# Kernel tuning notes

Hardware: AMD Instinct MI355X
Metric: run time of the kernel (lower is better)

The kernel has to match this reference:

```python
import jax, jax.numpy as jnp
import numpy as np

N = 100000
E = 1600000
F_IN = 32
HID = 16
C_OUT = 10
K = 4


def setup_inputs() -> dict:
    key = jax.random.key(0)
    k1, k2, k3, k4, k5, k6, k7 = jax.random.split(key, 7)
    x = jax.random.normal(k1, (N, F_IN), dtype=jnp.float32)
    edge_index = jax.random.randint(k2, (2, E), 0, N, dtype=jnp.int64)
    # ChebConv weights: one [in, out] matrix per Chebyshev order k
    W1 = jax.random.normal(k3, (K, F_IN, HID), dtype=jnp.float32) / np.sqrt(F_IN)
    b1 = jax.random.normal(k4, (HID,), dtype=jnp.float32) * 0.01
    W2 = jax.random.normal(k5, (K, HID, C_OUT), dtype=jnp.float32) / np.sqrt(HID)
    b2 = jax.random.normal(k6, (C_OUT,), dtype=jnp.float32) * 0.01
    return {"x": x, "edge_index": edge_index, "W1": W1, "b1": b1, "W2": W2, "b2": b2}


def _cheb_conv(h, src, dst, norm, W, b, num_nodes):
    # Tx_0 = h; Tx_1 = L_hat h; Tx_k = 2 L_hat Tx_{k-1} - Tx_{k-2}
    def prop(v):  # v: [N, F] -> L_hat v via sparse gather/scatter
        return jax.ops.segment_sum(norm[:, None] * v[src], dst, num_segments=num_nodes)

    Tx0 = h
    out = Tx0 @ W[0]
    Tx1 = prop(h)
    out = out + Tx1 @ W[1]
    for k in range(2, W.shape[0]):
        Tx2 = 2.0 * prop(Tx1) - Tx0
        out = out + Tx2 @ W[k]
        Tx0, Tx1 = Tx1, Tx2
    return out + b


def reference(x, edge_index, W1, b1, W2, b2):
    src, dst = edge_index[0], edge_index[1]
    num_nodes = x.shape[0]
    # symmetric normalization with lambda_max = 2: L_hat = -D^{-1/2} A D^{-1/2}
    deg = jax.ops.segment_sum(jnp.ones((src.shape[0],), dtype=x.dtype), dst, num_segments=num_nodes)
    dis = jnp.where(deg > 0, jax.lax.rsqrt(jnp.maximum(deg, 1.0)), 0.0)
    norm = -dis[src] * dis[dst]
    h = _cheb_conv(x, src, dst, norm, W1, b1, num_nodes)
    h = jax.nn.relu(h)
    # dropout is identity in eval mode
    h = _cheb_conv(h, src, dst, norm, W2, b2, num_nodes)
    return jax.nn.log_softmax(h, axis=1)
```

## Files before the change

### kernel.cpp

```cpp
#include <hip/hip_runtime.h>
#include <hip/hip_bf16.h>
#include <math.h>


#define BLK 256
#define BLKP 512
#define NBUCK_MAX 256
#define CHUNK 8192
#define CAPB 16384
#define PLACE_CAP 10240

__device__ inline unsigned short f32_to_bf16_rne(float f) {
    unsigned int u = __float_as_uint(f);
    unsigned int rounding = 0x7FFFu + ((u >> 16) & 1u);
    return (unsigned short)((u + rounding) >> 16);
}
__device__ inline unsigned int pack_bf16x2(float a, float b) {
    return (unsigned int)f32_to_bf16_rne(a) | ((unsigned int)f32_to_bf16_rne(b) << 16);
}
__device__ inline void unpack8(const uint4 u, float* f) {
    const unsigned int* p = &u.x;
#pragma unroll
    for (int j = 0; j < 4; j++) {
        unsigned int w = p[j];
        f[2 * j]     = __uint_as_float(w << 16);
        f[2 * j + 1] = __uint_as_float(w & 0xFFFF0000u);
    }
}
__device__ inline void add8(const uint4 u, float* acc) {
    const unsigned int* p = &u.x;
#pragma unroll
    for (int j = 0; j < 4; j++) {
        unsigned int w = p[j];
        acc[2 * j]     += __uint_as_float(w << 16);
        acc[2 * j + 1] += __uint_as_float(w & 0xFFFF0000u);
    }
}
__device__ inline uint4 pack8(const float* r) {
    uint4 o;
    o.x = pack_bf16x2(r[0], r[1]);
    o.y = pack_bf16x2(r[2], r[3]);
    o.z = pack_bf16x2(r[4], r[5]);
    o.w = pack_bf16x2(r[6], r[7]);
    return o;
}

__device__ inline void fma8_w8(const uint4 u, float s, const float* __restrict__ W,
                               float* acc) {
    const unsigned int* p = &u.x;
#pragma unroll
    for (int q = 0; q < 4; q++) {
        float fa = __uint_as_float(p[q] << 16) * s;
        float fb = __uint_as_float(p[q] & 0xFFFF0000u) * s;
        const float* Wa = W + (2 * q) * 16;
        const float* Wb = W + (2 * q + 1) * 16;
#pragma unroll
        for (int j = 0; j < 8; j++) acc[j] += fa * Wa[j] + fb * Wb[j];
    }
}
__device__ inline void fma8_w10(const uint4 u, float s, const float* __restrict__ W,
                                float* acc) {
    const unsigned int* p = &u.x;
#pragma unroll
    for (int q = 0; q < 4; q++) {
        float fa = __uint_as_float(p[q] << 16) * s;
        float fb = __uint_as_float(p[q] & 0xFFFF0000u) * s;
        const float* Wa = W + (2 * q) * 10;
        const float* Wb = W + (2 * q + 1) * 10;
#pragma unroll
        for (int j = 0; j < 10; j++) acc[j] += fa * Wa[j] + fb * Wb[j];
    }
}

__global__ __launch_bounds__(BLK)
void binned_scatter_kernel(const int* __restrict__ src, const int* __restrict__ dst,
                           int* __restrict__ bfill, int* __restrict__ tmp,
                           int E, int nbuck) {
    __shared__ int cnt[NBUCK_MAX];
    __shared__ int lofs[NBUCK_MAX + 1];
    __shared__ int pos[NBUCK_MAX];
    __shared__ int gbase[NBUCK_MAX];
    __shared__ int stage[CHUNK];
    __shared__ unsigned char bkt[CHUNK];

    int tid = threadIdx.x;
    int e0 = blockIdx.x * CHUNK;
    int nE = min(CHUNK, E - e0);

    for (int b = tid; b < nbuck; b += BLK) { cnt[b] = 0; pos[b] = 0; }
    __syncthreads();

    for (int i = tid; i < nE; i += BLK) {
        int d = dst[e0 + i];
        atomicAdd(&cnt[d >> 9], 1);
    }
    __syncthreads();

    {
        int v = (tid < nbuck) ? cnt[tid] : 0;
        lofs[tid] = v;
        __syncthreads();
        for (int off = 1; off < BLK; off <<= 1) {
            int t = (tid >= off) ? lofs[tid - off] : 0;
            __syncthreads();
            lofs[tid] += t;
            __syncthreads();
        }
        int incl = lofs[tid];
        __syncthreads();
        lofs[tid] = incl - v;
        if (tid == 0) lofs[nbuck] = nE;
        if (tid < nbuck && v > 0)
            gbase[tid] = tid * CAPB + atomicAdd(&bfill[tid], v);
    }
    __syncthreads();

    for (int i = tid; i < nE; i += BLK) {
        int s = src[e0 + i];
        int d = dst[e0 + i];
        int b = d >> 9;
        int slot = lofs[b] + atomicAdd(&pos[b], 1);
        stage[slot] = (s << 9) | (d & 511);
        bkt[slot] = (unsigned char)b;
    }
    __syncthreads();

    for (int i = tid; i < nE; i += BLK) {
        int b = bkt[i];
        tmp[gbase[b] + (i - lofs[b])] = stage[i];
    }
}

__global__ __launch_bounds__(BLKP)
void bucket_place_kernel(const int* __restrict__ bfill, const int* __restrict__ tmp,
                         int* __restrict__ psrc, int* __restrict__ rowbeg,
                         int* __restrict__ rowend, float* __restrict__ dis,
                         float* __restrict__ d2, float* __restrict__ inv,
                         const float* __restrict__ x, uint4* __restrict__ u0, int N) {
    __shared__ int cnt4[512 * 4];
    __shared__ int ofs[512];
    __shared__ int fill4[512 * 4];
    __shared__ int stage[PLACE_CAP];

    int b = blockIdx.x;
    int tid = threadIdx.x;
    int n0 = b << 9;
    int nn = min(512, N - n0);
    int S = b * CAPB;
    int tot = bfill[b];

    int t1 = N >> 2, t2 = N >> 1, t3 = t2 + t1;

    for (int i = tid; i < 512 * 4; i += BLKP) { cnt4[i] = 0; fill4[i] = 0; }
    __syncthreads();

    for (int i = tid; i < tot; i += BLKP) {
        int rec = tmp[S + i];
        int nl = rec & 511;
        int s = rec >> 9;
        int q = (s >= t2) ? ((s >= t3) ? 3 : 2) : ((s >= t1) ? 1 : 0);
        atomicAdd(&cnt4[nl * 4 + q], 1);
    }
    __syncthreads();

    int c0 = cnt4[tid * 4 + 0], c1 = cnt4[tid * 4 + 1];
    int c2 = cnt4[tid * 4 + 2], c3 = cnt4[tid * 4 + 3];
    int v = c0 + c1 + c2 + c3;
    cnt4[tid * 4 + 0] = 0;
    cnt4[tid * 4 + 1] = c0;
    cnt4[tid * 4 + 2] = c0 + c1;
    cnt4[tid * 4 + 3] = c0 + c1 + c2;
    ofs[tid] = v;
    __syncthreads();
    for (int off = 1; off < 512; off <<= 1) {
        int t = (tid >= off) ? ofs[tid - off] : 0;
        __syncthreads();
        ofs[tid] += t;
        __syncthreads();
    }
    int excl = ofs[tid] - v;
    __syncthreads();
    ofs[tid] = excl;
    float dn = (v > 0) ? rsqrtf((float)v) : 0.0f;
    if (tid < nn) {
        int n = n0 + tid;
        rowbeg[n] = S + excl;
        rowend[n] = S + excl + v;
        float fv = (float)v;
        dis[n] = dn;
        d2[n]  = (v > 0) ? 1.0f / fv : 0.0f;
        inv[n] = (v > 0) ? sqrtf(fv) : 0.0f;
        const float4* xr = reinterpret_cast<const float4*>(x + (size_t)n * 32);
#pragma unroll
        for (int c = 0; c < 4; c++) {
            float4 a = xr[c * 2], bb = xr[c * 2 + 1];
            float r[8] = {dn * a.x, dn * a.y, dn * a.z, dn * a.w,
                          dn * bb.x, dn * bb.y, dn * bb.z, dn * bb.w};
            u0[(size_t)n * 4 + c] = pack8(r);
        }
    }
    __syncthreads();

    if (tot <= PLACE_CAP) {
        for (int i = tid; i < tot; i += BLKP) {
            int rec = tmp[S + i];
            int nl = rec & 511;
            int s = rec >> 9;
            int q = (s >= t2) ? ((s >= t3) ? 3 : 2) : ((s >= t1) ? 1 : 0);
            int slot = ofs[nl] + cnt4[nl * 4 + q] + atomicAdd(&fill4[nl * 4 + q], 1);
            stage[slot] = s;
        }
        __syncthreads();
        for (int i = tid; i < tot; i += BLKP) psrc[S + i] = stage[i];
    } else {
        for (int i = tid; i < tot; i += BLKP) {
            int rec = tmp[S + i];
            int nl = rec & 511;
            int s = rec >> 9;
            int q = (s >= t2) ? ((s >= t3) ? 3 : 2) : ((s >= t1) ? 1 : 0);
            int slot = S + ofs[nl] + cnt4[nl * 4 + q] + atomicAdd(&fill4[nl * 4 + q], 1);
            psrc[slot] = s;
        }
    }
}

template <int C, bool HAVE_PREV>
__global__ __launch_bounds__(BLK)
void prop_u_kernel(const int* __restrict__ rowbeg, const int* __restrict__ rowend,
                   const int* __restrict__ psrc, const float* __restrict__ d2,
                   const uint4* __restrict__ vb, const uint4* __restrict__ prevb,
                   uint4* __restrict__ outb, float scale, int N) {
    int t = blockIdx.x * blockDim.x + threadIdx.x;
    int n = t / C;
    int c = t % C;
    if (n >= N) return;
    int beg = rowbeg[n];
    int end = rowend[n];
    float acc[8];
#pragma unroll
    for (int j = 0; j < 8; j++) acc[j] = 0.f;
    int i = beg;
    for (; i + 7 < end; i += 8) {
        int s0 = psrc[i],     s1 = psrc[i + 1], s2 = psrc[i + 2], s3 = psrc[i + 3];
        int s4 = psrc[i + 4], s5 = psrc[i + 5], s6 = psrc[i + 6], s7 = psrc[i + 7];
        uint4 a0 = vb[(size_t)s0 * C + c];
        uint4 a1 = vb[(size_t)s1 * C + c];
        uint4 a2 = vb[(size_t)s2 * C + c];
        uint4 a3 = vb[(size_t)s3 * C + c];
        uint4 a4 = vb[(size_t)s4 * C + c];
        uint4 a5 = vb[(size_t)s5 * C + c];
        uint4 a6 = vb[(size_t)s6 * C + c];
        uint4 a7 = vb[(size_t)s7 * C + c];
        add8(a0, acc); add8(a1, acc); add8(a2, acc); add8(a3, acc);
        add8(a4, acc); add8(a5, acc); add8(a6, acc); add8(a7, acc);
    }
    for (; i + 3 < end; i += 4) {
        int s0 = psrc[i], s1 = psrc[i + 1], s2 = psrc[i + 2], s3 = psrc[i + 3];
        uint4 a0 = vb[(size_t)s0 * C + c];
        uint4 a1 = vb[(size_t)s1 * C + c];
        uint4 a2 = vb[(size_t)s2 * C + c];
        uint4 a3 = vb[(size_t)s3 * C + c];
        add8(a0, acc); add8(a1, acc); add8(a2, acc); add8(a3, acc);
    }
    for (; i < end; i++) {
        uint4 a0 = vb[(size_t)psrc[i] * C + c];
        add8(a0, acc);
    }
    float f = -scale * d2[n];
    float r[8];
    if (HAVE_PREV) {
        float p[8];
        unpack8(prevb[(size_t)n * C + c], p);
#pragma unroll
        for (int j = 0; j < 8; j++) r[j] = f * acc[j] - p[j];
    } else {
#pragma unroll
        for (int j = 0; j < 8; j++) r[j] = f * acc[j];
    }
    outb[(size_t)n * C + c] = pack8(r);
}

__global__ __launch_bounds__(BLK)
void combine1_kernel(const float* __restrict__ x, const uint4* __restrict__ u1,
                     const uint4* __restrict__ u2, const uint4* __restrict__ u3,
                     const float* __restrict__ inv, const float* __restrict__ dis,
                     const float* __restrict__ W1, const float* __restrict__ b1,
                     uint4* __restrict__ hb, uint4* __restrict__ uh, int N) {
    __shared__ float sW[4 * 32 * 16];
    __shared__ float sb[16];
    for (int i = threadIdx.x; i < 4 * 32 * 16; i += blockDim.x) sW[i] = W1[i];
    if (threadIdx.x < 16) sb[threadIdx.x] = b1[threadIdx.x];
    __syncthreads();
    int t = blockIdx.x * blockDim.x + threadIdx.x;
    int n = t >> 1;
    int h = t & 1;
    if (n >= N) return;
    const float* sWh = sW + h * 8;
    float acc[8];
#pragma unroll
    for (int j = 0; j < 8; j++) acc[j] = sb[h * 8 + j];
    {
        const float4* in4 = reinterpret_cast<const float4*>(x + (size_t)n * 32);
#pragma unroll
        for (int q = 0; q < 8; q++) {
            float4 a = in4[q];
            const float* Wq = sWh + q * 4 * 16;
#pragma unroll
            for (int j = 0; j < 8; j++)
                acc[j] += a.x * Wq[j] + a.y * Wq[16 + j] + a.z * Wq[32 + j] + a.w * Wq[48 + j];
        }
    }
    float iv = inv[n];
#pragma unroll
    for (int c = 0; c < 4; c++) fma8_w8(u1[(size_t)n * 4 + c], iv, sWh + 512 + c * 128, acc);
#pragma unroll
    for (int c = 0; c < 4; c++) fma8_w8(u2[(size_t)n * 4 + c], iv, sWh + 1024 + c * 128, acc);
#pragma unroll
    for (int c = 0; c < 4; c++) fma8_w8(u3[(size_t)n * 4 + c], iv, sWh + 1536 + c * 128, acc);
    if (iv == 0.0f) {
        const float4* in4 = reinterpret_cast<const float4*>(x + (size_t)n * 32);
#pragma unroll
        for (int q = 0; q < 8; q++) {
            float4 a = in4[q];
            const float* Wq = sWh + 1024 + q * 4 * 16;
#pragma unroll
            for (int j = 0; j < 8; j++)
                acc[j] -= a.x * Wq[j] + a.y * Wq[16 + j] + a.z * Wq[32 + j] + a.w * Wq[48 + j];
        }
    }
    float dn = dis[n];
    float r[8], u[8];
#pragma unroll
    for (int j = 0; j < 8; j++) {
        r[j] = fmaxf(acc[j], 0.0f);
        u[j] = dn * r[j];
    }
    hb[(size_t)n * 2 + h] = pack8(r);
    uh[(size_t)n * 2 + h] = pack8(u);
}

__global__ __launch_bounds__(BLK)
void combine2_kernel(const uint4* __restrict__ hb, const uint4* __restrict__ us1,
                     const uint4* __restrict__ us2, const uint4* __restrict__ us3,
                     const float* __restrict__ inv,
                     const float* __restrict__ W2, const float* __restrict__ b2,
                     float* __restrict__ out, int N) {
    __shared__ float sW[4 * 16 * 10];
    __shared__ float sb[10];
    for (int i = threadIdx.x; i < 4 * 16 * 10; i += blockDim.x) sW[i] = W2[i];
    if (threadIdx.x < 10) sb[threadIdx.x] = b2[threadIdx.x];
    __syncthreads();
    int n = blockIdx.x * blockDim.x + threadIdx.x;
    if (n >= N) return;
    float acc[10];
#pragma unroll
    for (int c = 0; c < 10; c++) acc[c] = sb[c];
    float iv = inv[n];
#pragma unroll
    for (int c = 0; c < 2; c++) fma8_w10(hb[(size_t)n * 2 + c],  1.0f, sW + c * 80, acc);
#pragma unroll
    for (int c = 0; c < 2; c++) fma8_w10(us1[(size_t)n * 2 + c], iv, sW + 160 + c * 80, acc);
#pragma unroll
    for (int c = 0; c < 2; c++) fma8_w10(us2[(size_t)n * 2 + c], iv, sW + 320 + c * 80, acc);
#pragma unroll
    for (int c = 0; c < 2; c++) fma8_w10(us3[(size_t)n * 2 + c], iv, sW + 480 + c * 80, acc);
    if (iv == 0.0f) {
#pragma unroll
        for (int c = 0; c < 2; c++) fma8_w10(hb[(size_t)n * 2 + c], -1.0f, sW + 320 + c * 80, acc);
    }
    float m = acc[0];
#pragma unroll
    for (int c = 1; c < 10; c++) m = fmaxf(m, acc[c]);
    float sum = 0.0f;
#pragma unroll
    for (int c = 0; c < 10; c++) sum += expf(acc[c] - m);
    float lse = m + logf(sum);
    float* o = out + (size_t)n * 10;
#pragma unroll
    for (int c = 0; c < 10; c++) o[c] = acc[c] - lse;
}

extern "C" void kernel_launch(void* const* d_in, const int* in_sizes, int n_in,
                              void* d_out, int out_size, void* d_ws, size_t ws_size,
                              hipStream_t stream) {
    const float* x  = (const float*)d_in[0];
    const int*   ei = (const int*)d_in[1];
    const float* W1 = (const float*)d_in[2];
    const float* b1 = (const float*)d_in[3];
    const float* W2 = (const float*)d_in[4];
    const float* b2 = (const float*)d_in[5];
    float* out = (float*)d_out;

    const int N = in_sizes[0] / 32;
    const int E = in_sizes[1] / 2;
    const int* src = ei;
    const int* dst = ei + E;

    const int nbuck = (N + 511) / 512;

    char* w = (char*)d_ws;
    int*   bfill  = (int*)w;              w += NBUCK_MAX * 4;
    int*   rowbeg = (int*)w;              w += (size_t)(N + 4) * 4;
    int*   rowend = (int*)w;              w += (size_t)(N + 4) * 4;
    float* dis    = (float*)w;            w += (size_t)N * 4;
    float* d2     = (float*)w;            w += (size_t)N * 4;
    float* inv    = (float*)w;            w += (size_t)N * 4;
    int*   tmp    = (int*)w;              w += (size_t)NBUCK_MAX * CAPB * 4;
    int*   psrc   = (int*)w;              w += (size_t)NBUCK_MAX * CAPB * 4;
    uint4* u0     = (uint4*)w;            w += (size_t)64 * N;
    uint4* u1     = (uint4*)w;            w += (size_t)64 * N;
    uint4* u2     = (uint4*)w;            w += (size_t)64 * N;
    uint4* u3     = (uint4*)w;            w += (size_t)64 * N;
    uint4* hb     = (uint4*)w;            w += (size_t)32 * N;
    uint4* uh     = (uint4*)w;            w += (size_t)32 * N;
    uint4* us1    = (uint4*)w;            w += (size_t)32 * N;
    uint4* us2    = (uint4*)w;            w += (size_t)32 * N;
    uint4* us3    = (uint4*)w;            w += (size_t)32 * N;

    int gN   = (N + BLK - 1) / BLK;
    int gN2  = (N * 2 + BLK - 1) / BLK;
    int gU32 = (N * 4 + BLK - 1) / BLK;
    int gU16 = (N * 2 + BLK - 1) / BLK;
    int gCH  = (E + CHUNK - 1) / CHUNK;

    hipMemsetAsync(bfill, 0, NBUCK_MAX * sizeof(int), stream);
    binned_scatter_kernel<<<gCH, BLK, 0, stream>>>(src, dst, bfill, tmp, E, nbuck);
    bucket_place_kernel<<<nbuck, BLKP, 0, stream>>>(bfill, tmp, psrc, rowbeg, rowend,
                                                    dis, d2, inv, x, u0, N);

    prop_u_kernel<4, false><<<gU32, BLK, 0, stream>>>(rowbeg, rowend, psrc, d2, u0, nullptr, u1, 1.0f, N);
    prop_u_kernel<4, true ><<<gU32, BLK, 0, stream>>>(rowbeg, rowend, psrc, d2, u1, u0,      u2, 2.0f, N);
    prop_u_kernel<4, true ><<<gU32, BLK, 0, stream>>>(rowbeg, rowend, psrc, d2, u2, u1,      u3, 2.0f, N);
    combine1_kernel<<<gN2, BLK, 0, stream>>>(x, u1, u2, u3, inv, dis, W1, b1, hb, uh, N);

    prop_u_kernel<2, false><<<gU16, BLK, 0, stream>>>(rowbeg, rowend, psrc, d2, uh,  nullptr, us1, 1.0f, N);
    prop_u_kernel<2, true ><<<gU16, BLK, 0, stream>>>(rowbeg, rowend, psrc, d2, us1, uh,      us2, 2.0f, N);
    prop_u_kernel<2, true ><<<gU16, BLK, 0, stream>>>(rowbeg, rowend, psrc, d2, us2, us1,     us3, 2.0f, N);
    combine2_kernel<<<gN, BLK, 0, stream>>>(hb, us1, us2, us3, inv, W2, b2, out, N);
}
```

Before: 280.2 us.

## Fuse last Chebyshev propagation into combine kernels with cross-lane reduction

The third propagation step of each ChebConv layer is merged into the following combine kernel. Each node is now handled by 4 (layer 1) or 2 (layer 2) lanes, one per feature chunk, and the partial matmul sums are reduced with xor shuffles. This removes two kernel launches and the write and re-read of the u3/us3 intermediates. In exchange, each lane does a 16- or 10-wide output accumulation with more registers, and the lanes sharing a node repeat the output-stage work.

```diff
diff --git a/kernel.cpp b/kernel.cpp
--- a/kernel.cpp
+++ b/kernel.cpp
@@ -43,33 +43,6 @@
     o.z = pack_bf16x2(r[4], r[5]);
     o.w = pack_bf16x2(r[6], r[7]);
     return o;
-}
-
-__device__ inline void fma8_w8(const uint4 u, float s, const float* __restrict__ W,
-                               float* acc) {
-    const unsigned int* p = &u.x;
-#pragma unroll
-    for (int q = 0; q < 4; q++) {
-        float fa = __uint_as_float(p[q] << 16) * s;
-        float fb = __uint_as_float(p[q] & 0xFFFF0000u) * s;
-        const float* Wa = W + (2 * q) * 16;
-        const float* Wb = W + (2 * q + 1) * 16;
-#pragma unroll
-        for (int j = 0; j < 8; j++) acc[j] += fa * Wa[j] + fb * Wb[j];
-    }
-}
-__device__ inline void fma8_w10(const uint4 u, float s, const float* __restrict__ W,
-                                float* acc) {
-    const unsigned int* p = &u.x;
-#pragma unroll
-    for (int q = 0; q < 4; q++) {
-        float fa = __uint_as_float(p[q] << 16) * s;
-        float fb = __uint_as_float(p[q] & 0xFFFF0000u) * s;
-        const float* Wa = W + (2 * q) * 10;
-        const float* Wb = W + (2 * q + 1) * 10;
-#pragma unroll
-        for (int j = 0; j < 10; j++) acc[j] += fa * Wa[j] + fb * Wb[j];
-    }
 }
 
 __global__ __launch_bounds__(BLK)
@@ -281,103 +254,177 @@
 }
 
 __global__ __launch_bounds__(BLK)
-void combine1_kernel(const float* __restrict__ x, const uint4* __restrict__ u1,
-                     const uint4* __restrict__ u2, const uint4* __restrict__ u3,
-                     const float* __restrict__ inv, const float* __restrict__ dis,
-                     const float* __restrict__ W1, const float* __restrict__ b1,
-                     uint4* __restrict__ hb, uint4* __restrict__ uh, int N) {
+void prop_combine1_kernel(const int* __restrict__ rowbeg, const int* __restrict__ rowend,
+                          const int* __restrict__ psrc, const float* __restrict__ d2,
+                          const uint4* __restrict__ u2t, const uint4* __restrict__ u1t,
+                          const float* __restrict__ x, const float* __restrict__ inv,
+                          const float* __restrict__ dis, const float* __restrict__ W1,
+                          const float* __restrict__ b1, uint4* __restrict__ hb,
+                          uint4* __restrict__ uh, int N) {
     __shared__ float sW[4 * 32 * 16];
     __shared__ float sb[16];
     for (int i = threadIdx.x; i < 4 * 32 * 16; i += blockDim.x) sW[i] = W1[i];
     if (threadIdx.x < 16) sb[threadIdx.x] = b1[threadIdx.x];
     __syncthreads();
     int t = blockIdx.x * blockDim.x + threadIdx.x;
-    int n = t >> 1;
-    int h = t & 1;
+    int n = t >> 2;
+    int c = t & 3;
     if (n >= N) return;
-    const float* sWh = sW + h * 8;
+    int beg = rowbeg[n];
+    int end = rowend[n];
     float acc[8];
 #pragma unroll
-    for (int j = 0; j < 8; j++) acc[j] = sb[h * 8 + j];
+    for (int j = 0; j < 8; j++) acc[j] = 0.f;
+    int i = beg;
+    for (; i + 7 < end; i += 8) {
+        int s0 = psrc[i],     s1 = psrc[i + 1], s2 = psrc[i + 2], s3 = psrc[i + 3];
+        int s4 = psrc[i + 4], s5 = psrc[i + 5], s6 = psrc[i + 6], s7 = psrc[i + 7];
+        uint4 a0 = u2t[(size_t)s0 * 4 + c];
+        uint4 a1 = u2t[(size_t)s1 * 4 + c];
+        uint4 a2 = u2t[(size_t)s2 * 4 + c];
+        uint4 a3 = u2t[(size_t)s3 * 4 + c];
+        uint4 a4 = u2t[(size_t)s4 * 4 + c];
+        uint4 a5 = u2t[(size_t)s5 * 4 + c];
+        uint4 a6 = u2t[(size_t)s6 * 4 + c];
+        uint4 a7 = u2t[(size_t)s7 * 4 + c];
+        add8(a0, acc); add8(a1, acc); add8(a2, acc); add8(a3, acc);
+        add8(a4, acc); add8(a5, acc); add8(a6, acc); add8(a7, acc);
+    }
+    for (; i < end; i++) add8(u2t[(size_t)psrc[i] * 4 + c], acc);
+    float f = -2.0f * d2[n];
+    float p1[8], p2[8], r[8];
+    unpack8(u1t[(size_t)n * 4 + c], p1);
+    unpack8(u2t[(size_t)n * 4 + c], p2);
+#pragma unroll
+    for (int j = 0; j < 8; j++) r[j] = f * acc[j] - p1[j];
+    float a16[16];
+#pragma unroll
+    for (int o = 0; o < 16; o++) a16[o] = (c == 0) ? sb[o] : 0.0f;
+    float iv = inv[n];
+    float xv[8];
     {
-        const float4* in4 = reinterpret_cast<const float4*>(x + (size_t)n * 32);
-#pragma unroll
-        for (int q = 0; q < 8; q++) {
-            float4 a = in4[q];
-            const float* Wq = sWh + q * 4 * 16;
-#pragma unroll
-            for (int j = 0; j < 8; j++)
-                acc[j] += a.x * Wq[j] + a.y * Wq[16 + j] + a.z * Wq[32 + j] + a.w * Wq[48 + j];
-        }
-    }
-    float iv = inv[n];
-#pragma unroll
-    for (int c = 0; c < 4; c++) fma8_w8(u1[(size_t)n * 4 + c], iv, sWh + 512 + c * 128, acc);
-#pragma unroll
-    for (int c = 0; c < 4; c++) fma8_w8(u2[(size_t)n * 4 + c], iv, sWh + 1024 + c * 128, acc);
-#pragma unroll
-    for (int c = 0; c < 4; c++) fma8_w8(u3[(size_t)n * 4 + c], iv, sWh + 1536 + c * 128, acc);
+        const float4* xr = reinterpret_cast<const float4*>(x + (size_t)n * 32 + c * 8);
+        float4 a = xr[0], bb = xr[1];
+        xv[0] = a.x; xv[1] = a.y; xv[2] = a.z; xv[3] = a.w;
+        xv[4] = bb.x; xv[5] = bb.y; xv[6] = bb.z; xv[7] = bb.w;
+    }
+    const float* W0 = sW + (c * 8) * 16;
+#pragma unroll
+    for (int j = 0; j < 8; j++) {
+        float w0 = xv[j];
+        float w1 = p1[j] * iv;
+        float w2 = p2[j] * iv;
+        float w3 = r[j] * iv;
+        const float* Wj = W0 + j * 16;
+#pragma unroll
+        for (int o = 0; o < 16; o++)
+            a16[o] += w0 * Wj[o] + w1 * Wj[512 + o] + w2 * Wj[1024 + o] + w3 * Wj[1536 + o];
+    }
     if (iv == 0.0f) {
-        const float4* in4 = reinterpret_cast<const float4*>(x + (size_t)n * 32);
-#pragma unroll
-        for (int q = 0; q < 8; q++) {
-            float4 a = in4[q];
-            const float* Wq = sWh + 1024 + q * 4 * 16;
-#pragma unroll
-            for (int j = 0; j < 8; j++)
-                acc[j] -= a.x * Wq[j] + a.y * Wq[16 + j] + a.z * Wq[32 + j] + a.w * Wq[48 + j];
-        }
+#pragma unroll
+        for (int j = 0; j < 8; j++) {
+            const float* Wj = W0 + j * 16 + 1024;
+#pragma unroll
+            for (int o = 0; o < 16; o++) a16[o] -= xv[j] * Wj[o];
+        }
+    }
+#pragma unroll
+    for (int m = 1; m <= 2; m <<= 1) {
+#pragma unroll
+        for (int o = 0; o < 16; o++) a16[o] += __shfl_xor(a16[o], m);
     }
     float dn = dis[n];
-    float r[8], u[8];
+    int half = c & 1;
+    float w8[8];
 #pragma unroll
     for (int j = 0; j < 8; j++) {
-        r[j] = fmaxf(acc[j], 0.0f);
-        u[j] = dn * r[j];
-    }
-    hb[(size_t)n * 2 + h] = pack8(r);
-    uh[(size_t)n * 2 + h] = pack8(u);
+        float v = fmaxf(a16[half * 8 + j], 0.0f);
+        w8[j] = (c < 2) ? v : dn * v;
+    }
+    if (c < 2) hb[(size_t)n * 2 + half] = pack8(w8);
+    else       uh[(size_t)n * 2 + half] = pack8(w8);
 }
 
 __global__ __launch_bounds__(BLK)
-void combine2_kernel(const uint4* __restrict__ hb, const uint4* __restrict__ us1,
-                     const uint4* __restrict__ us2, const uint4* __restrict__ us3,
-                     const float* __restrict__ inv,
-                     const float* __restrict__ W2, const float* __restrict__ b2,
-                     float* __restrict__ out, int N) {
+void prop_combine2_kernel(const int* __restrict__ rowbeg, const int* __restrict__ rowend,
+                          const int* __restrict__ psrc, const float* __restrict__ d2,
+                          const uint4* __restrict__ us2t, const uint4* __restrict__ us1t,
+                          const uint4* __restrict__ hbt, const float* __restrict__ inv,
+                          const float* __restrict__ W2, const float* __restrict__ b2,
+                          float* __restrict__ out, int N) {
     __shared__ float sW[4 * 16 * 10];
     __shared__ float sb[10];
     for (int i = threadIdx.x; i < 4 * 16 * 10; i += blockDim.x) sW[i] = W2[i];
     if (threadIdx.x < 10) sb[threadIdx.x] = b2[threadIdx.x];
     __syncthreads();
-    int n = blockIdx.x * blockDim.x + threadIdx.x;
+    int t = blockIdx.x * blockDim.x + threadIdx.x;
+    int n = t >> 1;
+    int c = t & 1;
     if (n >= N) return;
-    float acc[10];
-#pragma unroll
-    for (int c = 0; c < 10; c++) acc[c] = sb[c];
+    int beg = rowbeg[n];
+    int end = rowend[n];
+    float acc[8];
+#pragma unroll
+    for (int j = 0; j < 8; j++) acc[j] = 0.f;
+    int i = beg;
+    for (; i + 7 < end; i += 8) {
+        int s0 = psrc[i],     s1 = psrc[i + 1], s2 = psrc[i + 2], s3 = psrc[i + 3];
+        int s4 = psrc[i + 4], s5 = psrc[i + 5], s6 = psrc[i + 6], s7 = psrc[i + 7];
+        uint4 a0 = us2t[(size_t)s0 * 2 + c];
+        uint4 a1 = us2t[(size_t)s1 * 2 + c];
+        uint4 a2 = us2t[(size_t)s2 * 2 + c];
+        uint4 a3 = us2t[(size_t)s3 * 2 + c];
+        uint4 a4 = us2t[(size_t)s4 * 2 + c];
+        uint4 a5 = us2t[(size_t)s5 * 2 + c];
+        uint4 a6 = us2t[(size_t)s6 * 2 + c];
+        uint4 a7 = us2t[(size_t)s7 * 2 + c];
+        add8(a0, acc); add8(a1, acc); add8(a2, acc); add8(a3, acc);
+        add8(a4, acc); add8(a5, acc); add8(a6, acc); add8(a7, acc);
+    }
+    for (; i < end; i++) add8(us2t[(size_t)psrc[i] * 2 + c], acc);
+    float f = -2.0f * d2[n];
+    float p1[8], p2[8], ph[8], r[8];
+    unpack8(us1t[(size_t)n * 2 + c], p1);
+    unpack8(us2t[(size_t)n * 2 + c], p2);
+    unpack8(hbt[(size_t)n * 2 + c], ph);
+#pragma unroll
+    for (int j = 0; j < 8; j++) r[j] = f * acc[j] - p1[j];
+    float a10[10];
+#pragma unroll
+    for (int o = 0; o < 10; o++) a10[o] = (c == 0) ? sb[o] : 0.0f;
     float iv = inv[n];
-#pragma unroll
-    for (int c = 0; c < 2; c++) fma8_w10(hb[(size_t)n * 2 + c],  1.0f, sW + c * 80, acc);
-#pragma unroll
-    for (int c = 0; c < 2; c++) fma8_w10(us1[(size_t)n * 2 + c], iv, sW + 160 + c * 80, acc);
-#pragma unroll
-    for (int c = 0; c < 2; c++) fma8_w10(us2[(size_t)n * 2 + c], iv, sW + 320 + c * 80, acc);
-#pragma unroll
-    for (int c = 0; c < 2; c++) fma8_w10(us3[(size_t)n * 2 + c], iv, sW + 480 + c * 80, acc);
+    const float* W0 = sW + (c * 8) * 10;
+#pragma unroll
+    for (int j = 0; j < 8; j++) {
+        float w0 = ph[j];
+        float w1 = p1[j] * iv;
+        float w2 = p2[j] * iv;
+        float w3 = r[j] * iv;
+        const float* Wj = W0 + j * 10;
+#pragma unroll
+        for (int o = 0; o < 10; o++)
+            a10[o] += w0 * Wj[o] + w1 * Wj[160 + o] + w2 * Wj[320 + o] + w3 * Wj[480 + o];
+    }
     if (iv == 0.0f) {
 #pragma unroll
-        for (int c = 0; c < 2; c++) fma8_w10(hb[(size_t)n * 2 + c], -1.0f, sW + 320 + c * 80, acc);
-    }
-    float m = acc[0];
-#pragma unroll
-    for (int c = 1; c < 10; c++) m = fmaxf(m, acc[c]);
+        for (int j = 0; j < 8; j++) {
+            const float* Wj = W0 + j * 10 + 320;
+#pragma unroll
+            for (int o = 0; o < 10; o++) a10[o] -= ph[j] * Wj[o];
+        }
+    }
+#pragma unroll
+    for (int o = 0; o < 10; o++) a10[o] += __shfl_xor(a10[o], 1);
+    float m = a10[0];
+#pragma unroll
+    for (int o = 1; o < 10; o++) m = fmaxf(m, a10[o]);
     float sum = 0.0f;
 #pragma unroll
-    for (int c = 0; c < 10; c++) sum += expf(acc[c] - m);
+    for (int o = 0; o < 10; o++) sum += expf(a10[o] - m);
     float lse = m + logf(sum);
-    float* o = out + (size_t)n * 10;
-#pragma unroll
-    for (int c = 0; c < 10; c++) o[c] = acc[c] - lse;
+    float* op = out + (size_t)n * 10 + c * 5;
+#pragma unroll
+    for (int o = 0; o < 5; o++) op[o] = a10[c * 5 + o] - lse;
 }
 
 extern "C" void kernel_launch(void* const* d_in, const int* in_sizes, int n_in,
@@ -410,15 +457,11 @@
     uint4* u0     = (uint4*)w;            w += (size_t)64 * N;
     uint4* u1     = (uint4*)w;            w += (size_t)64 * N;
     uint4* u2     = (uint4*)w;            w += (size_t)64 * N;
-    uint4* u3     = (uint4*)w;            w += (size_t)64 * N;
     uint4* hb     = (uint4*)w;            w += (size_t)32 * N;
     uint4* uh     = (uint4*)w;            w += (size_t)32 * N;
     uint4* us1    = (uint4*)w;            w += (size_t)32 * N;
     uint4* us2    = (uint4*)w;            w += (size_t)32 * N;
-    uint4* us3    = (uint4*)w;            w += (size_t)32 * N;
-
-    int gN   = (N + BLK - 1) / BLK;
-    int gN2  = (N * 2 + BLK - 1) / BLK;
+
     int gU32 = (N * 4 + BLK - 1) / BLK;
     int gU16 = (N * 2 + BLK - 1) / BLK;
     int gCH  = (E + CHUNK - 1) / CHUNK;
@@ -430,11 +473,11 @@
 
     prop_u_kernel<4, false><<<gU32, BLK, 0, stream>>>(rowbeg, rowend, psrc, d2, u0, nullptr, u1, 1.0f, N);
     prop_u_kernel<4, true ><<<gU32, BLK, 0, stream>>>(rowbeg, rowend, psrc, d2, u1, u0,      u2, 2.0f, N);
-    prop_u_kernel<4, true ><<<gU32, BLK, 0, stream>>>(rowbeg, rowend, psrc, d2, u2, u1,      u3, 2.0f, N);
-    combine1_kernel<<<gN2, BLK, 0, stream>>>(x, u1, u2, u3, inv, dis, W1, b1, hb, uh, N);
+    prop_combine1_kernel<<<gU32, BLK, 0, stream>>>(rowbeg, rowend, psrc, d2, u2, u1,
+                                                   x, inv, dis, W1, b1, hb, uh, N);
 
     prop_u_kernel<2, false><<<gU16, BLK, 0, stream>>>(rowbeg, rowend, psrc, d2, uh,  nullptr, us1, 1.0f, N);
     prop_u_kernel<2, true ><<<gU16, BLK, 0, stream>>>(rowbeg, rowend, psrc, d2, us1, uh,      us2, 2.0f, N);
-    prop_u_kernel<2, true ><<<gU16, BLK, 0, stream>>>(rowbeg, rowend, psrc, d2, us2, us1,     us3, 2.0f, N);
-    combine2_kernel<<<gN, BLK, 0, stream>>>(hb, us1, us2, us3, inv, W2, b2, out, N);
-}
+    prop_combine2_kernel<<<gU16, BLK, 0, stream>>>(rowbeg, rowend, psrc, d2, us2, us1,
+                                                   hb, inv, W2, b2, out, N);
+}
```

Result: slower. 295.6 us (+5.5%).
